# Kernel tuning notes

Measured on AMD Instinct MI355X. Metric: run time of the kernel, lower is better.

Reference implementation:

```python
import jax, jax.numpy as jnp
import numpy as np

NUM_CLASSES = 1000
TEMPERATURE = 0.1
B, B_OOD, D = 4096, 4096, 512


def _l2norm(x):
    return x / jnp.linalg.norm(x, axis=-1, keepdims=True)


def setup_inputs() -> dict:
    key = jax.random.key(0)
    k1, k2, k3, k4, k5 = jax.random.split(key, 5)
    return {
        "centers1": _l2norm(jax.random.normal(k1, (NUM_CLASSES, D), dtype=jnp.float32)),
        "features": _l2norm(jax.random.normal(k2, (B, D), dtype=jnp.float32)),
        "targets": jax.random.randint(k3, (B,), 0, NUM_CLASSES, dtype=jnp.int64 if jax.config.jax_enable_x64 else jnp.int32),
        "features_ood": _l2norm(jax.random.normal(k4, (B_OOD, D), dtype=jnp.float32)),
        "pseudo_target_ood": jax.random.randint(k5, (B_OOD,), 0, NUM_CLASSES, dtype=jnp.int64 if jax.config.jax_enable_x64 else jnp.int32),
    }


def reference(centers1, features, targets, features_ood, pseudo_target_ood):
    C = centers1.shape[0]
    b = features.shape[0]
    bo = features_ood.shape[0]
    n = b + C + bo  # total anchors: batch + class centers + ood

    centers_lbl = jnp.arange(C, dtype=targets.dtype)
    ood_lbl = jnp.full((bo,), C, dtype=targets.dtype)  # ood gets label == num_classes
    targets_all = jnp.concatenate([targets, centers_lbl, ood_lbl])              # [N]
    targets_all_class = jnp.concatenate([targets, centers_lbl, pseudo_target_ood])  # [N]

    # per-class count over all N labels (pseudo labels for ood)
    batch_cls_count = jnp.zeros((C,), dtype=jnp.float32).at[targets_all_class].add(1.0)

    # positive mask: same label as anchor, excluding self (diagonal for j < B)
    mask = (targets_all[:b, None] == targets_all[None, :]).astype(jnp.float32)  # [B,N]
    logits_mask = 1.0 - (jnp.arange(n)[None, :] == jnp.arange(b)[:, None]).astype(jnp.float32)
    mask = mask * logits_mask

    features_all = jnp.concatenate([features, centers1, features_ood], axis=0)  # [N,D]
    logits = jnp.matmul(features, features_all.T) / TEMPERATURE                 # [B,N]
    logits = logits - jax.lax.stop_gradient(jnp.max(logits, axis=1, keepdims=True))

    exp_logits = jnp.exp(logits) * logits_mask
    # class-balanced per-instance weight (count of the column's class, minus positive mask)
    per_ins_weight = batch_cls_count[targets_all_class][None, :] - mask         # [B,N]
    exp_logits_sum = jnp.sum(exp_logits / per_ins_weight, axis=1, keepdims=True)
    log_prob = logits - jnp.log(exp_logits_sum)

    mean_log_prob_pos = jnp.sum(mask * log_prob, axis=1) / jnp.sum(mask, axis=1)
    loss = -jnp.mean(mean_log_prob_pos)
    return loss
```

## Files before the change

### kernel.cpp

```cpp
#include <hip/hip_runtime.h>
#include <stdint.h>

#define NUM_C 1000
#define NB    4096
#define NCOL  9192
#define NPAD  9216
#define DK    512
#define BM    128
#define BN    256
#define INV_T 10.0f

typedef __attribute__((ext_vector_type(16))) float f32x16;
typedef __attribute__((ext_vector_type(8)))  int   i32x8;

#define OFF_FALL  0u
#define OFF_CNT   4718592u
#define OFF_CNTT  4722688u
#define OFF_S     4726784u
#define OFF_P     4743168u

#define NCHUNKBLK 1152

__device__ __forceinline__ void async16(const void* g, void* l) {
  __builtin_amdgcn_global_load_lds((const __attribute__((address_space(1))) void*)g,
                                   (__attribute__((address_space(3))) void*)l,
                                   16, 0, 0);
}

__device__ __forceinline__ unsigned sw_e4m3(float x) {
  float ax = fabsf(x);
  unsigned s = (__float_as_uint(x) >> 24) & 0x80u;
  if (ax < 0.015625f) {
    int n = (int)rintf(ax * 512.0f);
    if (n >= 8) return s | 0x08u;
    return s | (unsigned)n;
  }
  if (ax >= 448.0f) return s | 0x7Eu;
  unsigned u = __float_as_uint(ax);
  int ee = (int)(u >> 23) - 127;
  float scale = __uint_as_float((unsigned)(3 - ee + 127) << 23);
  int qv = (int)rintf(ax * scale);
  if (qv == 16) { ee++; qv = 8; }
  return s | (unsigned)(((ee + 7) << 3) | (qv - 8));
}

template <bool HI>
__device__ __forceinline__ int cvt2(float a, float b, int old) {
#if __has_builtin(__builtin_amdgcn_cvt_pk_fp8_f32)
  return __builtin_amdgcn_cvt_pk_fp8_f32(a, b, old, HI);
#else
  unsigned pk = sw_e4m3(a) | (sw_e4m3(b) << 8);
  return HI ? (int)(((unsigned)old & 0x0000FFFFu) | (pk << 16))
            : (int)(((unsigned)old & 0xFFFF0000u) | pk);
#endif
}

__device__ __forceinline__ i32x8 mk8(uint4 lo, uint4 hi) {
  i32x8 r;
  r[0] = (int)lo.x; r[1] = (int)lo.y; r[2] = (int)lo.z; r[3] = (int)lo.w;
  r[4] = (int)hi.x; r[5] = (int)hi.y; r[6] = (int)hi.z; r[7] = (int)hi.w;
  return r;
}

#define MFMA_SC(a, b, c) \
  __builtin_amdgcn_mfma_scale_f32_32x32x64_f8f6f4((a), (b), (c), 0, 0, 0, 0x7F7F7F7F, 0, 0x7F7F7F7F)

__global__ __launch_bounds__(256) void prep_k(const float* __restrict__ centers,
                                              const float* __restrict__ feats,
                                              const float* __restrict__ ood,
                                              const int* __restrict__ targets,
                                              const int* __restrict__ pseudo,
                                              uint4* __restrict__ fall,
                                              unsigned* __restrict__ cnt,
                                              unsigned* __restrict__ cntT,
                                              float* __restrict__ SP) {
  __shared__ unsigned hc[1024];
  __shared__ unsigned hct[1024];
  const int tid = threadIdx.x;

  if (blockIdx.x > 0) {
    int idx  = (blockIdx.x - 1) * 256 + tid;
    int tile = idx >> 10;
    int kq   = (idx >> 7) & 7;
    int p    = idx & 127;
    int c    = p ^ ((p >> 3) & 7);
    int lane = c >> 1;
    int row  = tile * 32 + (lane & 31);
    int k0   = kq * 64 + (lane >> 5) * 32 + (c & 1) * 16;

    const float* src = nullptr;
    if (row < NB)              src = feats   + (size_t)row * DK;
    else if (row < NB + NUM_C) src = centers + (size_t)(row - NB) * DK;
    else if (row < NCOL)       src = ood     + (size_t)(row - NB - NUM_C) * DK;
    uint4 out = make_uint4(0u, 0u, 0u, 0u);
    if (src) {
      float4 v0 = *(const float4*)(src + k0);
      float4 v1 = *(const float4*)(src + k0 + 4);
      float4 v2 = *(const float4*)(src + k0 + 8);
      float4 v3 = *(const float4*)(src + k0 + 12);
      int q;
      q = 0; q = cvt2<false>(v0.x, v0.y, q); q = cvt2<true>(v0.z, v0.w, q); out.x = (unsigned)q;
      q = 0; q = cvt2<false>(v1.x, v1.y, q); q = cvt2<true>(v1.z, v1.w, q); out.y = (unsigned)q;
      q = 0; q = cvt2<false>(v2.x, v2.y, q); q = cvt2<true>(v2.z, v2.w, q); out.z = (unsigned)q;
      q = 0; q = cvt2<false>(v3.x, v3.y, q); q = cvt2<true>(v3.z, v3.w, q); out.w = (unsigned)q;
    }
    fall[idx] = out;

    if (blockIdx.x <= 32)
      SP[(blockIdx.x - 1) * 256 + tid] = 0.0f;
  } else {
    for (int kk = tid; kk < 1024; kk += 256) { hc[kk] = 0u; hct[kk] = 0u; }
    __syncthreads();
    for (int i = tid; i < NB; i += 256) {
      int tt = targets[i];
      atomicAdd(&hc[tt], 1u);
      atomicAdd(&hct[tt], 1u);
      atomicAdd(&hc[pseudo[i]], 1u);
    }
    __syncthreads();
    for (int kk = tid; kk < 1024; kk += 256) {
      cnt[kk]  = hc[kk];
      cntT[kk] = hct[kk];
    }
  }
}

__global__ __launch_bounds__(512, 4) void gemm_fused(const unsigned char* __restrict__ fall,
                                                     const int* __restrict__ targets,
                                                     const int* __restrict__ pseudo,
                                                     const unsigned* __restrict__ cnt,
                                                     float* __restrict__ Sacc,
                                                     float* __restrict__ Pacc) {
  __shared__ unsigned char Alds[65536];
  __shared__ int4   sTab[BN];
  __shared__ int    sTgt[BM];
  __shared__ float  sS[BM];
  __shared__ float  sP[BM];

  const int tid  = threadIdx.x;
  int flat = (int)blockIdx.y * 36 + (int)blockIdx.x;
  int swz  = (flat & 7) * 144 + (flat >> 3);
  const int nTile = swz >> 5;
  const int mTile = swz & 31;
  const int lane  = tid & 63;
  const int wv    = tid >> 6;
  const int wm    = wv >> 2;
  const int wn    = wv & 3;

  {
    const unsigned char* aSrc = fall + (size_t)mTile * 65536;
#pragma unroll
    for (int i = 0; i < 8; i++)
      async16(aSrc + (i * 512 + tid) * 16, &Alds[(i * 512 + tid) * 16]);
  }

  if (tid < BN) {
    int j = nTile * BN + tid;
    int lbl, tac;
    if (j >= NCOL)         { lbl = -1; tac = -1; }
    else if (j < NB)       { tac = targets[j]; lbl = tac; }
    else if (j < NB+NUM_C) { tac = j - NB;     lbl = tac; }
    else                   { tac = pseudo[j - NB - NUM_C]; lbl = NUM_C; }
    float r0 = 0.f, r1 = 0.f;
    if (tac >= 0) {
      float w = (float)(1u + cnt[tac]);
      r0 = 1.0f / w;
      r1 = 1.0f / (w - 1.0f);
    }
    sTab[tid] = make_int4(lbl, __float_as_int(r0), __float_as_int(r1), 0);
  } else if (tid < BN + BM) {
    int i = tid - BN;
    sTgt[i] = targets[mTile * BM + i];
    sS[i] = 0.f;
    sP[i] = 0.f;
  }

  f32x16 acc00, acc01, acc10, acc11;
  {
    f32x16 z;
#pragma unroll
    for (int t = 0; t < 16; t++) z[t] = 0.f;
    acc00 = z; acc01 = z; acc10 = z; acc11 = z;
  }

  const int swzo = ((lane >> 2) & 7) << 4;
  const int off0 = (lane << 5) ^ swzo;
  const int off1 = off0 ^ 16;

  const unsigned char* bBase0 = fall + (size_t)(nTile * 8 + wn * 2) * 16384;
  const unsigned char* bBase1 = bBase0 + 16384;

  uint4 bb[2][4];
#pragma unroll
  for (int s = 0; s < 2; s++) {
    const unsigned char* pb0 = bBase0 + s * 2048;
    const unsigned char* pb1 = bBase1 + s * 2048;
    bb[s][0] = *(const uint4*)(pb0 + off0);
    bb[s][1] = *(const uint4*)(pb0 + off1);
    bb[s][2] = *(const uint4*)(pb1 + off0);
    bb[s][3] = *(const uint4*)(pb1 + off1);
  }

  __syncthreads();

#pragma unroll
  for (int kq = 0; kq < 8; kq++) {
    const int sl = kq & 1;
    i32x8 bf0 = mk8(bb[sl][0], bb[sl][1]);
    i32x8 bf1 = mk8(bb[sl][2], bb[sl][3]);
    if (kq < 6) {
      const unsigned char* pb0 = bBase0 + (kq + 2) * 2048;
      const unsigned char* pb1 = bBase1 + (kq + 2) * 2048;
      bb[sl][0] = *(const uint4*)(pb0 + off0);
      bb[sl][1] = *(const uint4*)(pb0 + off1);
      bb[sl][2] = *(const uint4*)(pb1 + off0);
      bb[sl][3] = *(const uint4*)(pb1 + off1);
    }
    {
      const unsigned ao = (unsigned)(wm * 2 + 0) * 16384u + (unsigned)kq * 2048u;
      uint4 al = *(const uint4*)&Alds[ao + off0];
      uint4 ah = *(const uint4*)&Alds[ao + off1];
      i32x8 af = mk8(al, ah);
      acc00 = MFMA_SC(bf0, af, acc00);
      acc01 = MFMA_SC(bf1, af, acc01);
    }
    {
      const unsigned ao = (unsigned)(wm * 2 + 1) * 16384u + (unsigned)kq * 2048u;
      uint4 al = *(const uint4*)&Alds[ao + off0];
      uint4 ah = *(const uint4*)&Alds[ao + off1];
      i32x8 af = mk8(al, ah);
      acc10 = MFMA_SC(bf0, af, acc10);
      acc11 = MFMA_SC(bf1, af, acc11);
    }
  }

  const int cq = lane & 31;
  const int hh = lane >> 5;
  const int iloc0 = wm * 64 + cq;
  const int iloc1 = iloc0 + 32;
  const int ig0 = mTile * BM + iloc0;
  const int ig1 = mTile * BM + iloc1;
  const int ti0 = sTgt[iloc0];
  const int ti1 = sTgt[iloc1];

  float s0 = 0.f, s1 = 0.f, p0 = 0.f, p1 = 0.f;
#pragma unroll
  for (int nj = 0; nj < 2; nj++) {
#pragma unroll
    for (int r = 0; r < 16; r++) {
      int jl = wn * 64 + nj * 32 + (r & 3) + 8 * (r >> 2) + 4 * hh;
      int jg = nTile * BN + jl;
      int4 tb = sTab[jl];
      float rw0 = __int_as_float(tb.y);
      float rw1 = __int_as_float(tb.z);
      float a0 = nj ? acc01[r] : acc00[r];
      float a1 = nj ? acc11[r] : acc10[r];
      {
        bool d = (jg == ig0);
        bool pp = (tb.x == ti0) && !d;
        float rw = d ? 0.f : (pp ? rw1 : rw0);
        float e = __expf(fmaf(a0, INV_T, -INV_T));
        s0 = fmaf(e, rw, s0);
        p0 += pp ? a0 : 0.f;
      }
      {
        bool d = (jg == ig1);
        bool pp = (tb.x == ti1) && !d;
        float rw = d ? 0.f : (pp ? rw1 : rw0);
        float e = __expf(fmaf(a1, INV_T, -INV_T));
        s1 = fmaf(e, rw, s1);
        p1 += pp ? a1 : 0.f;
      }
    }
  }
  atomicAdd(&sS[iloc0], s0);
  atomicAdd(&sP[iloc0], p0 * INV_T);
  atomicAdd(&sS[iloc1], s1);
  atomicAdd(&sP[iloc1], p1 * INV_T);

  __syncthreads();
  if (tid < BM) {
    int ig = mTile * BM + tid;
    atomicAdd(&Sacc[ig], sS[tid]);
    atomicAdd(&Pacc[ig], sP[tid]);
  }
}

__global__ __launch_bounds__(256) void finalize_k(const float* __restrict__ S,
                                                  const float* __restrict__ P,
                                                  const int* __restrict__ targets,
                                                  const unsigned* __restrict__ cntT,
                                                  float* __restrict__ out) {
  __shared__ unsigned ct[1024];
  __shared__ float red[4];
  int tid = threadIdx.x;
  for (int k = tid; k < 1024; k += 256) ct[k] = cntT[k];
  __syncthreads();
  float local = 0.f;
  for (int i = tid; i < NB; i += 256) {
    float npos = (float)ct[targets[i]];
    local += P[i] / npos - INV_T - __logf(S[i]);
  }
  for (int m = 1; m < 64; m <<= 1) local += __shfl_xor(local, m, 64);
  if ((tid & 63) == 0) red[tid >> 6] = local;
  __syncthreads();
  if (tid == 0) {
    float t = red[0] + red[1] + red[2] + red[3];
    out[0] = -t / (float)NB;
  }
}

extern "C" void kernel_launch(void* const* d_in, const int* in_sizes, int n_in,
                              void* d_out, int out_size, void* d_ws, size_t ws_size,
                              hipStream_t stream) {
  const float* centers = (const float*)d_in[0];
  const float* feats   = (const float*)d_in[1];
  const int*   targets = (const int*)d_in[2];
  const float* ood     = (const float*)d_in[3];
  const int*   pseudo  = (const int*)d_in[4];

  char* ws = (char*)d_ws;
  uint4*    fall  = (uint4*)(ws + OFF_FALL);
  unsigned* cnt   = (unsigned*)(ws + OFF_CNT);
  unsigned* cntT  = (unsigned*)(ws + OFF_CNTT);
  float*    Sacc  = (float*)(ws + OFF_S);
  float*    Pacc  = (float*)(ws + OFF_P);

  prep_k<<<dim3(NCHUNKBLK + 1), 256, 0, stream>>>(centers, feats, ood, targets, pseudo,
                                                  fall, cnt, cntT, Sacc);
  gemm_fused<<<dim3(NPAD / BN, NB / BM), 512, 0, stream>>>((const unsigned char*)fall, targets,
                                                           pseudo, cnt, Sacc, Pacc);
  finalize_k<<<1, 256, 0, stream>>>(Sacc, Pacc, targets, cntT, (float*)d_out);
}
```

Before: 125.2 us.

## Process two N tiles per block reusing the staged A tile

```diff
diff --git a/kernel.cpp b/kernel.cpp
--- a/kernel.cpp
+++ b/kernel.cpp
@@ -138,14 +138,15 @@
   __shared__ float  sP[BM];
 
   const int tid  = threadIdx.x;
-  int flat = (int)blockIdx.y * 36 + (int)blockIdx.x;
-  int swz  = (flat & 7) * 144 + (flat >> 3);
-  const int nTile = swz >> 5;
-  const int mTile = swz & 31;
-  const int lane  = tid & 63;
-  const int wv    = tid >> 6;
-  const int wm    = wv >> 2;
-  const int wn    = wv & 3;
+  int flat = (int)blockIdx.x;
+  int swz  = (flat & 7) * 72 + (flat >> 3);
+  const int mTile  = swz & 31;
+  const int nT0    = swz >> 5;
+  const int nT1    = nT0 + 18;
+  const int lane   = tid & 63;
+  const int wv     = tid >> 6;
+  const int wm     = wv >> 2;
+  const int wn     = wv & 3;
 
   {
     const unsigned char* aSrc = fall + (size_t)mTile * 65536;
@@ -154,20 +155,28 @@
       async16(aSrc + (i * 512 + tid) * 16, &Alds[(i * 512 + tid) * 16]);
   }
 
+  int lblB = -1; float r0B = 0.f, r1B = 0.f;
   if (tid < BN) {
-    int j = nTile * BN + tid;
+    int j = nT0 * BN + tid;
     int lbl, tac;
-    if (j >= NCOL)         { lbl = -1; tac = -1; }
-    else if (j < NB)       { tac = targets[j]; lbl = tac; }
+    if (j < NB)            { tac = targets[j]; lbl = tac; }
     else if (j < NB+NUM_C) { tac = j - NB;     lbl = tac; }
     else                   { tac = pseudo[j - NB - NUM_C]; lbl = NUM_C; }
-    float r0 = 0.f, r1 = 0.f;
-    if (tac >= 0) {
-      float w = (float)(1u + cnt[tac]);
-      r0 = 1.0f / w;
-      r1 = 1.0f / (w - 1.0f);
+    float w  = (float)(1u + cnt[tac]);
+    float r0 = 1.0f / w;
+    float r1 = 1.0f / (w - 1.0f);
+    sTab[tid] = make_int4(lbl, __float_as_int(r0), __float_as_int(r1), 0);
+    j = nT1 * BN + tid;
+    int tac1;
+    if (j >= NCOL)         { lblB = -1; tac1 = -1; }
+    else if (j < NB)       { tac1 = targets[j]; lblB = tac1; }
+    else if (j < NB+NUM_C) { tac1 = j - NB;     lblB = tac1; }
+    else                   { tac1 = pseudo[j - NB - NUM_C]; lblB = NUM_C; }
+    if (tac1 >= 0) {
+      float w1 = (float)(1u + cnt[tac1]);
+      r0B = 1.0f / w1;
+      r1B = 1.0f / (w1 - 1.0f);
     }
-    sTab[tid] = make_int4(lbl, __float_as_int(r0), __float_as_int(r1), 0);
   } else if (tid < BN + BM) {
     int i = tid - BN;
     sTgt[i] = targets[mTile * BM + i];
@@ -175,115 +184,139 @@
     sP[i] = 0.f;
   }
 
-  f32x16 acc00, acc01, acc10, acc11;
-  {
-    f32x16 z;
-#pragma unroll
-    for (int t = 0; t < 16; t++) z[t] = 0.f;
-    acc00 = z; acc01 = z; acc10 = z; acc11 = z;
-  }
-
   const int swzo = ((lane >> 2) & 7) << 4;
   const int off0 = (lane << 5) ^ swzo;
   const int off1 = off0 ^ 16;
 
-  const unsigned char* bBase0 = fall + (size_t)(nTile * 8 + wn * 2) * 16384;
-  const unsigned char* bBase1 = bBase0 + 16384;
+  const unsigned char* b0T0 = fall + (size_t)(nT0 * 8 + wn * 2) * 16384;
+  const unsigned char* b1T0 = b0T0 + 16384;
+  const unsigned char* b0T1 = fall + (size_t)(nT1 * 8 + wn * 2) * 16384;
+  const unsigned char* b1T1 = b0T1 + 16384;
 
   uint4 bb[2][4];
 #pragma unroll
   for (int s = 0; s < 2; s++) {
-    const unsigned char* pb0 = bBase0 + s * 2048;
-    const unsigned char* pb1 = bBase1 + s * 2048;
-    bb[s][0] = *(const uint4*)(pb0 + off0);
-    bb[s][1] = *(const uint4*)(pb0 + off1);
-    bb[s][2] = *(const uint4*)(pb1 + off0);
-    bb[s][3] = *(const uint4*)(pb1 + off1);
-  }
-
-  __syncthreads();
-
+    const unsigned char* p0 = b0T0 + s * 2048;
+    const unsigned char* p1 = b1T0 + s * 2048;
+    bb[s][0] = *(const uint4*)(p0 + off0);
+    bb[s][1] = *(const uint4*)(p0 + off1);
+    bb[s][2] = *(const uint4*)(p1 + off0);
+    bb[s][3] = *(const uint4*)(p1 + off1);
+  }
+
+  f32x16 acc00, acc01, acc10, acc11;
+  f32x16 z;
 #pragma unroll
-  for (int kq = 0; kq < 8; kq++) {
-    const int sl = kq & 1;
-    i32x8 bf0 = mk8(bb[sl][0], bb[sl][1]);
-    i32x8 bf1 = mk8(bb[sl][2], bb[sl][3]);
-    if (kq < 6) {
-      const unsigned char* pb0 = bBase0 + (kq + 2) * 2048;
-      const unsigned char* pb1 = bBase1 + (kq + 2) * 2048;
-      bb[sl][0] = *(const uint4*)(pb0 + off0);
-      bb[sl][1] = *(const uint4*)(pb0 + off1);
-      bb[sl][2] = *(const uint4*)(pb1 + off0);
-      bb[sl][3] = *(const uint4*)(pb1 + off1);
-    }
-    {
-      const unsigned ao = (unsigned)(wm * 2 + 0) * 16384u + (unsigned)kq * 2048u;
-      uint4 al = *(const uint4*)&Alds[ao + off0];
-      uint4 ah = *(const uint4*)&Alds[ao + off1];
-      i32x8 af = mk8(al, ah);
-      acc00 = MFMA_SC(bf0, af, acc00);
-      acc01 = MFMA_SC(bf1, af, acc01);
-    }
-    {
-      const unsigned ao = (unsigned)(wm * 2 + 1) * 16384u + (unsigned)kq * 2048u;
-      uint4 al = *(const uint4*)&Alds[ao + off0];
-      uint4 ah = *(const uint4*)&Alds[ao + off1];
-      i32x8 af = mk8(al, ah);
-      acc10 = MFMA_SC(bf0, af, acc10);
-      acc11 = MFMA_SC(bf1, af, acc11);
-    }
-  }
-
-  const int cq = lane & 31;
-  const int hh = lane >> 5;
-  const int iloc0 = wm * 64 + cq;
-  const int iloc1 = iloc0 + 32;
-  const int ig0 = mTile * BM + iloc0;
-  const int ig1 = mTile * BM + iloc1;
-  const int ti0 = sTgt[iloc0];
-  const int ti1 = sTgt[iloc1];
-
-  float s0 = 0.f, s1 = 0.f, p0 = 0.f, p1 = 0.f;
-#pragma unroll
-  for (int nj = 0; nj < 2; nj++) {
-#pragma unroll
-    for (int r = 0; r < 16; r++) {
-      int jl = wn * 64 + nj * 32 + (r & 3) + 8 * (r >> 2) + 4 * hh;
-      int jg = nTile * BN + jl;
-      int4 tb = sTab[jl];
-      float rw0 = __int_as_float(tb.y);
-      float rw1 = __int_as_float(tb.z);
-      float a0 = nj ? acc01[r] : acc00[r];
-      float a1 = nj ? acc11[r] : acc10[r];
-      {
-        bool d = (jg == ig0);
-        bool pp = (tb.x == ti0) && !d;
-        float rw = d ? 0.f : (pp ? rw1 : rw0);
-        float e = __expf(fmaf(a0, INV_T, -INV_T));
-        s0 = fmaf(e, rw, s0);
-        p0 += pp ? a0 : 0.f;
-      }
-      {
-        bool d = (jg == ig1);
-        bool pp = (tb.x == ti1) && !d;
-        float rw = d ? 0.f : (pp ? rw1 : rw0);
-        float e = __expf(fmaf(a1, INV_T, -INV_T));
-        s1 = fmaf(e, rw, s1);
-        p1 += pp ? a1 : 0.f;
-      }
-    }
-  }
-  atomicAdd(&sS[iloc0], s0);
-  atomicAdd(&sP[iloc0], p0 * INV_T);
-  atomicAdd(&sS[iloc1], s1);
-  atomicAdd(&sP[iloc1], p1 * INV_T);
-
+  for (int t = 0; t < 16; t++) z[t] = 0.f;
+  acc00 = z; acc01 = z; acc10 = z; acc11 = z;
+
+  __syncthreads();
+
+#define KLOOP(C0, C1, N0, N1)                                              \
+  _Pragma("unroll")                                                        \
+  for (int kq = 0; kq < 8; kq++) {                                         \
+    const int sl = kq & 1;                                                 \
+    i32x8 bf0 = mk8(bb[sl][0], bb[sl][1]);                                 \
+    i32x8 bf1 = mk8(bb[sl][2], bb[sl][3]);                                 \
+    {                                                                      \
+      const unsigned char* p0 = (kq < 6) ? (C0) + (kq + 2) * 2048          \
+                                         : (N0) + (kq - 6) * 2048;         \
+      const unsigned char* p1 = (kq < 6) ? (C1) + (kq + 2) * 2048          \
+                                         : (N1) + (kq - 6) * 2048;         \
+      bb[sl][0] = *(const uint4*)(p0 + off0);                              \
+      bb[sl][1] = *(const uint4*)(p0 + off1);                              \
+      bb[sl][2] = *(const uint4*)(p1 + off0);                              \
+      bb[sl][3] = *(const uint4*)(p1 + off1);                              \
+    }                                                                      \
+    {                                                                      \
+      const unsigned ao = (unsigned)(wm * 2 + 0) * 16384u + (unsigned)kq * 2048u; \
+      uint4 al = *(const uint4*)&Alds[ao + off0];                          \
+      uint4 ah = *(const uint4*)&Alds[ao + off1];                          \
+      i32x8 af = mk8(al, ah);                                              \
+      acc00 = MFMA_SC(bf0, af, acc00);                                     \
+      acc01 = MFMA_SC(bf1, af, acc01);                                     \
+    }                                                                      \
+    {                                                                      \
+      const unsigned ao = (unsigned)(wm * 2 + 1) * 16384u + (unsigned)kq * 2048u; \
+      uint4 al = *(const uint4*)&Alds[ao + off0];                          \
+      uint4 ah = *(const uint4*)&Alds[ao + off1];                          \
+      i32x8 af = mk8(al, ah);                                              \
+      acc10 = MFMA_SC(bf0, af, acc10);                                     \
+      acc11 = MFMA_SC(bf1, af, acc11);                                     \
+    }                                                                      \
+  }
+
+#define EPILOGUE(NT)                                                       \
+  {                                                                        \
+    const int cq = lane & 31;                                              \
+    const int hh = lane >> 5;                                              \
+    const int iloc0 = wm * 64 + cq;                                        \
+    const int iloc1 = iloc0 + 32;                                          \
+    const int ig0 = mTile * BM + iloc0;                                    \
+    const int ig1 = mTile * BM + iloc1;                                    \
+    const int ti0 = sTgt[iloc0];                                           \
+    const int ti1 = sTgt[iloc1];                                           \
+    float s0 = 0.f, s1 = 0.f, p0a = 0.f, p1a = 0.f;                        \
+    _Pragma("unroll")                                                      \
+    for (int nj = 0; nj < 2; nj++) {                                       \
+      _Pragma("unroll")                                                    \
+      for (int r = 0; r < 16; r++) {                                       \
+        int jl = wn * 64 + nj * 32 + (r & 3) + 8 * (r >> 2) + 4 * hh;      \
+        int jg = (NT) * BN + jl;                                           \
+        int4 tb = sTab[jl];                                                \
+        float rw0 = __int_as_float(tb.y);                                  \
+        float rw1 = __int_as_float(tb.z);                                  \
+        float a0 = nj ? acc01[r] : acc00[r];                               \
+        float a1 = nj ? acc11[r] : acc10[r];                               \
+        {                                                                  \
+          bool d = (jg == ig0);                                            \
+          bool pp = (tb.x == ti0) && !d;                                   \
+          float rw = d ? 0.f : (pp ? rw1 : rw0);                           \
+          float e = __expf(fmaf(a0, INV_T, -INV_T));                       \
+          s0 = fmaf(e, rw, s0);                                            \
+          p0a += pp ? a0 : 0.f;                                            \
+        }                                                                  \
+        {                                                                  \
+          bool d = (jg == ig1);                                            \
+          bool pp = (tb.x == ti1) && !d;                                   \
+          float rw = d ? 0.f : (pp ? rw1 : rw0);                           \
+          float e = __expf(fmaf(a1, INV_T, -INV_T));                       \
+          s1 = fmaf(e, rw, s1);                                            \
+          p1a += pp ? a1 : 0.f;                                            \
+        }                                                                  \
+      }                                                                    \
+    }                                                                      \
+    atomicAdd(&sS[iloc0], s0);                                             \
+    atomicAdd(&sP[iloc0], p0a * INV_T);                                    \
+    atomicAdd(&sS[iloc1], s1);                                             \
+    atomicAdd(&sP[iloc1], p1a * INV_T);                                    \
+  }
+
+  KLOOP(b0T0, b1T0, b0T1, b1T1)
+  EPILOGUE(nT0)
   __syncthreads();
   if (tid < BM) {
     int ig = mTile * BM + tid;
     atomicAdd(&Sacc[ig], sS[tid]);
     atomicAdd(&Pacc[ig], sP[tid]);
-  }
+    sS[tid] = 0.f;
+    sP[tid] = 0.f;
+  }
+  if (tid < BN)
+    sTab[tid] = make_int4(lblB, __float_as_int(r0B), __float_as_int(r1B), 0);
+  acc00 = z; acc01 = z; acc10 = z; acc11 = z;
+  __syncthreads();
+
+  KLOOP(b0T1, b1T1, b0T1, b1T1)
+  EPILOGUE(nT1)
+  __syncthreads();
+  if (tid < BM) {
+    int ig = mTile * BM + tid;
+    atomicAdd(&Sacc[ig], sS[tid]);
+    atomicAdd(&Pacc[ig], sP[tid]);
+  }
+#undef KLOOP
+#undef EPILOGUE
 }
 
 __global__ __launch_bounds__(256) void finalize_k(const float* __restrict__ S,
@@ -328,7 +361,7 @@
 
   prep_k<<<dim3(NCHUNKBLK + 1), 256, 0, stream>>>(centers, feats, ood, targets, pseudo,
                                                   fall, cnt, cntT, Sacc);
-  gemm_fused<<<dim3(NPAD / BN, NB / BM), 512, 0, stream>>>((const unsigned char*)fall, targets,
-                                                           pseudo, cnt, Sacc, Pacc);
+  gemm_fused<<<dim3(576), 512, 0, stream>>>((const unsigned char*)fall, targets,
+                                            pseudo, cnt, Sacc, Pacc);
   finalize_k<<<1, 256, 0, stream>>>(Sacc, Pacc, targets, cntT, (float*)d_out);
 }
```

Result: slower. 192.5 us (+53.8%).
